# Kernel optimization log

Hardware: AMD Instinct MI355X
Metric: run time of the kernel (lower is better)

Reference implementation:

```python
import jax, jax.numpy as jnp
import numpy as np

STRIDES = (4, 8, 16, 32, 64)
SIZES = (32.0, 64.0, 128.0, 256.0, 512.0)
RATIOS = (0.5, 1.0, 2.0)
IM_H, IM_W = 1024, 1024
PRE_NMS = 1000
POST_NMS = 1000
IOU_THRESH = 0.7
MIN_SIZE = 0.0
SCALE_CLAMP = float(np.log(1000.0 / 16.0))  # detectron2 delta clamp


def _anchors(stride, size, H, W):
    # detectron2-style: area-preserving anchors centered on stride grid
    r = jnp.asarray(RATIOS, jnp.float32)
    w = jnp.sqrt(size * size / r)
    h = w * r
    base = jnp.stack([-w / 2, -h / 2, w / 2, h / 2], axis=1)  # [A,4]
    sx = jnp.arange(W, dtype=jnp.float32) * stride
    sy = jnp.arange(H, dtype=jnp.float32) * stride
    yy, xx = jnp.meshgrid(sy, sx, indexing='ij')
    shifts = jnp.stack([xx, yy, xx, yy], axis=-1).reshape(-1, 1, 4)  # [H*W,1,4]
    return (shifts + base[None]).reshape(-1, 4)  # [H*W*A, 4]


def _conv(x, w, b, pad):
    y = jax.lax.conv_general_dilated(
        x, w, (1, 1), [(pad, pad), (pad, pad)],
        dimension_numbers=('NCHW', 'OIHW', 'NCHW'))
    return y + b[None, :, None, None]


def _decode_clip(deltas, anchors):
    # deltas [N,M,4], anchors [1,M,4] -> clipped xyxy boxes [N,M,4]
    wa = anchors[..., 2] - anchors[..., 0]
    ha = anchors[..., 3] - anchors[..., 1]
    cxa = anchors[..., 0] + 0.5 * wa
    cya = anchors[..., 1] + 0.5 * ha
    dx, dy = deltas[..., 0], deltas[..., 1]
    dw = jnp.minimum(deltas[..., 2], SCALE_CLAMP)
    dh = jnp.minimum(deltas[..., 3], SCALE_CLAMP)
    cx = dx * wa + cxa
    cy = dy * ha + cya
    w = jnp.exp(dw) * wa
    h = jnp.exp(dh) * ha
    x1 = jnp.clip(cx - 0.5 * w, 0.0, float(IM_W))
    y1 = jnp.clip(cy - 0.5 * h, 0.0, float(IM_H))
    x2 = jnp.clip(cx + 0.5 * w, 0.0, float(IM_W))
    y2 = jnp.clip(cy + 0.5 * h, 0.0, float(IM_H))
    return jnp.stack([x1, y1, x2, y2], axis=-1)


def _iou_matrix(boxes):
    x1, y1, x2, y2 = boxes[:, 0], boxes[:, 1], boxes[:, 2], boxes[:, 3]
    area = (x2 - x1) * (y2 - y1)
    ix1 = jnp.maximum(x1[:, None], x1[None, :])
    iy1 = jnp.maximum(y1[:, None], y1[None, :])
    ix2 = jnp.minimum(x2[:, None], x2[None, :])
    iy2 = jnp.minimum(y2[:, None], y2[None, :])
    inter = jnp.clip(ix2 - ix1, 0.0) * jnp.clip(iy2 - iy1, 0.0)
    return inter / jnp.maximum(area[:, None] + area[None, :] - inter, 1e-6)


def _nms_keep(boxes):
    # boxes [M,4] already sorted by descending score; greedy NMS keep mask
    M = boxes.shape[0]
    valid = ((boxes[:, 2] - boxes[:, 0]) >= MIN_SIZE) & \
            ((boxes[:, 3] - boxes[:, 1]) >= MIN_SIZE)
    iou = _iou_matrix(boxes)
    idx = jnp.arange(M)

    def body(i, keep):
        sup = keep[i] & (iou[i] > IOU_THRESH) & (idx > i)
        return keep & ~sup

    return jax.lax.fori_loop(0, M, body, valid)


def _nms_single(boxes, scores):
    # boxes [PRE_NMS,4] score-sorted desc -> [POST_NMS,4], zero-padded
    del scores  # already sorted by score
    keep = _nms_keep(jax.lax.stop_gradient(boxes))
    order = jnp.argsort(~keep, stable=True)  # kept boxes first, score order preserved
    kept = keep[order][:POST_NMS]
    out = boxes[order[:POST_NMS]] * kept[:, None].astype(boxes.dtype)
    return out


def _rpn_forward(feats, conv_w, conv_b, obj_w, obj_b, delta_w, delta_b):
    N = feats[0].shape[0]
    A = len(RATIOS)
    boxes_all, scores_all = [], []
    for lvl, x in enumerate(feats):
        H, W = x.shape[2], x.shape[3]
        t = jax.nn.relu(_conv(x, conv_w, conv_b, 1))            # [N,256,H,W]
        logit = jax.nn.sigmoid(_conv(t, obj_w, obj_b, 0))       # [N,A,H,W]
        reg = _conv(t, delta_w, delta_b, 0)                     # [N,4A,H,W]
        scores = logit.transpose(0, 2, 3, 1).reshape(N, -1)     # [N,H*W*A]
        deltas = reg.reshape(N, A, 4, H, W).transpose(0, 3, 4, 1, 2).reshape(N, -1, 4)
        anchors = _anchors(STRIDES[lvl], SIZES[lvl], H, W)      # [H*W*A,4]
        rois = _decode_clip(deltas, anchors[None])              # [N,H*W*A,4]
        k = min(PRE_NMS, scores.shape[1])
        top_s, top_i = jax.lax.top_k(scores, k)
        boxes_all.append(jnp.take_along_axis(rois, top_i[..., None], axis=1))
        scores_all.append(top_s)
    boxes = jnp.concatenate(boxes_all, axis=1)   # [N,T,4]
    scores = jnp.concatenate(scores_all, axis=1)  # [N,T]
    top_s, top_i = jax.lax.top_k(scores, PRE_NMS)
    top_b = jnp.take_along_axis(boxes, top_i[..., None], axis=1)  # [N,PRE_NMS,4]
    dets = jax.vmap(_nms_single)(top_b, top_s)   # [N,POST_NMS,4]
    batch_inds = jnp.zeros((N, POST_NMS, 1), dets.dtype)
    ret = jnp.concatenate([batch_inds, dets], axis=2).reshape(-1, 5)
    return ret, dets.reshape(-1, 4)


def setup_inputs() -> dict:
    key = jax.random.key(0)
    ks = jax.random.split(key, 11)
    C = 256
    shapes = [(2, C, 256, 256), (2, C, 128, 128), (2, C, 64, 64),
              (2, C, 32, 32), (2, C, 16, 16)]
    inp = {}
    for i, (name, s) in enumerate(zip(['p2', 'p3', 'p4', 'p5', 'p6'], shapes)):
        inp[name] = jax.random.normal(ks[i], s, jnp.float32)
    inp['conv_w'] = jax.random.normal(ks[5], (C, C, 3, 3), jnp.float32) * 0.02
    inp['conv_b'] = jnp.zeros((C,), jnp.float32)
    inp['obj_w'] = jax.random.normal(ks[6], (3, C, 1, 1), jnp.float32) * 0.05
    inp['obj_b'] = jnp.zeros((3,), jnp.float32)
    inp['delta_w'] = jax.random.normal(ks[7], (12, C, 1, 1), jnp.float32) * 0.05
    inp['delta_b'] = jnp.zeros((12,), jnp.float32)
    return inp


def reference(p2, p3, p4, p5, p6, conv_w, conv_b, obj_w, obj_b, delta_w, delta_b):
    return _rpn_forward((p2, p3, p4, p5, p6), conv_w, conv_b,
                        obj_w, obj_b, delta_w, delta_b)
```

## Files before the change

kernel.cpp:

```cpp
#include <hip/hip_runtime.h>
#include <stdint.h>

typedef unsigned long long u64;
typedef unsigned int u32;
typedef _Float16 f16;
typedef _Float16 f16x8 __attribute__((ext_vector_type(8)));
typedef float f32x4 __attribute__((ext_vector_type(4)));
typedef u32 u32x4 __attribute__((ext_vector_type(4)));

#define NA 261888
#define CAP 4096
#define SCALE_CLAMP 4.135166556742356f
#define NBLK_IMG 684

#define WT_OFF   0
#define BOX_OFF  2359296
#define SB_OFF   10739712
#define HIST_OFF 12834816
#define FINE_OFF 12867584
#define META_OFF 13359104
#define CAND_OFF 13359168
#define TOP_OFF  13424704
#define MASK_OFF 13456704
#define NH_OFF   13712704
#define WS_NEED  192494912ull

#define E_WH   0
#define E_HB   3840
#define E_PART 3872
#define BUFB   26112

#define AS1C(p) ((const __attribute__((address_space(1))) void*)(p))
#define AS3(p)  ((__attribute__((address_space(3))) void*)(p))

__global__ void k_wprep(const float* __restrict__ w, f16* __restrict__ wHL) {
    int i = blockIdx.x * 256 + threadIdx.x;
    if (i >= 589824) return;
    int co = i / 2304, rem = i % 2304;
    int ci = rem / 9, kyx = rem % 9;
    float v = w[i];
    f16 h = (f16)v;
    f16 lo = (f16)(v - (float)h);
    u32 idx = (u32)((kyx * 32 + (ci >> 3)) * 256 + co) * 8 + (ci & 7);
    wHL[idx] = h;
    wHL[589824 + idx] = lo;
}

__global__ __launch_bounds__(256) void k_nhwc(
    const float* __restrict__ p2, const float* __restrict__ p3,
    const float* __restrict__ p4, const float* __restrict__ p5,
    const float* __restrict__ p6, unsigned char* __restrict__ nh)
{
    int t = blockIdx.x * 256 + threadIdx.x;
    if (t >= 1396736) return;
    int n = t / 698368;
    int r = t % 698368;
    int lvl, c, pxy, HW, cumpx;
    const float* in;
    if (r < 524288)      { lvl = 0; HW = 65536; cumpx = 0;     c = r >> 16; pxy = r & 65535; in = p2; }
    else if (r < 655360) { lvl = 1; HW = 16384; cumpx = 65536; r -= 524288; c = r >> 14; pxy = r & 16383; in = p3; }
    else if (r < 688128) { lvl = 2; HW = 4096;  cumpx = 81920; r -= 655360; c = r >> 12; pxy = r & 4095;  in = p4; }
    else if (r < 696320) { lvl = 3; HW = 1024;  cumpx = 86016; r -= 688128; c = r >> 10; pxy = r & 1023;  in = p5; }
    else                 { lvl = 4; HW = 256;   cumpx = 87040; r -= 696320; c = r >> 8;  pxy = r & 255;   in = p6; }
    (void)lvl;
    const float* gp = in + ((size_t)n * 256 + (size_t)c * 32) * HW + pxy;
    u32 hi[16], lo[16];
#pragma unroll
    for (int k = 0; k < 16; ++k) {
        float v0 = gp[(size_t)(2 * k) * HW];
        float v1 = gp[(size_t)(2 * k + 1) * HW];
        f16 h0 = (f16)v0, h1 = (f16)v1;
        f16 e0 = (f16)(v0 - (float)h0), e1 = (f16)(v1 - (float)h1);
        hi[k] = ((u32)__builtin_bit_cast(unsigned short, h1) << 16) |
                 (u32)__builtin_bit_cast(unsigned short, h0);
        lo[k] = ((u32)__builtin_bit_cast(unsigned short, e1) << 16) |
                 (u32)__builtin_bit_cast(unsigned short, e0);
    }
    unsigned char* dst = nh + ((size_t)n * 87296 + (size_t)cumpx) * 1024
                            + ((size_t)c * HW + (size_t)pxy) * 128;
    u32x4* d4 = (u32x4*)dst;
#pragma unroll
    for (int i = 0; i < 4; ++i)
        d4[i] = (u32x4){hi[4 * i], hi[4 * i + 1], hi[4 * i + 2], hi[4 * i + 3]};
#pragma unroll
    for (int i = 0; i < 4; ++i)
        d4[4 + i] = (u32x4){lo[4 * i], lo[4 * i + 1], lo[4 * i + 2], lo[4 * i + 3]};
}

__global__ __launch_bounds__(256, 2) void k_conv_nh(
    const unsigned char* __restrict__ nh, const f16* __restrict__ wHL,
    const float* __restrict__ cb, const float* __restrict__ ow,
    const float* __restrict__ ob, const float* __restrict__ dw_,
    const float* __restrict__ db_, u32* __restrict__ scoreb,
    float* __restrict__ boxes)
{
    __shared__ __align__(16) float smf[13056];
    char* smemc = (char*)smf;

    int tid = threadIdx.x;
    int bid = blockIdx.x;
    int ebid = (bid & 7) * 171 + (bid >> 3);
    int n = ebid / NBLK_IMG;
    int tb = ebid % NBLK_IMG;
    int lvl, t0, cumpx;
    if      (tb < 512) { lvl = 0; t0 = tb;       cumpx = 0;     }
    else if (tb < 640) { lvl = 1; t0 = tb - 512; cumpx = 65536; }
    else if (tb < 672) { lvl = 2; t0 = tb - 640; cumpx = 81920; }
    else if (tb < 680) { lvl = 3; t0 = tb - 672; cumpx = 86016; }
    else               { lvl = 4; t0 = tb - 680; cumpx = 87040; }
    int H = 256 >> lvl, W = H;
    int HW = H * W;
    int xtiles = (W >= 32) ? (W >> 5) : 1;
    int xt = t0 % xtiles, yt = t0 / xtiles;
    int tx0 = xt * 32, ty0 = yt * 4;
    const unsigned char* nhb = nh + ((size_t)n * 87296 + (size_t)cumpx) * 1024;

    int l = tid & 63;
    int wid = tid >> 6;
    int wm = wid >> 1, wn = wid & 1;
    int lr = l & 15;
    int lg = l >> 4;

    int srco[7];
#pragma unroll
    for (int w = 0; w < 7; ++w) {
        int flat = w * 256 + tid;
        int px = flat >> 3, seg = flat & 7;
        int dy = px / 34, dx = px % 34;
        int y = ty0 + dy - 1, x = tx0 + dx - 1;
        bool part = flat < 1632;
        bool inb = part && y >= 0 && y < H && x >= 0 && x < W;
        srco[w] = inb ? ((y * W + x) * 128 + ((seg * 16) ^ ((px & 7) << 4))) : -1;
    }

#pragma unroll
    for (int w = 0; w < 7; ++w) {
        int flat = w * 256 + tid;
        if (flat < 1632 && srco[w] < 0) {
            *(u32x4*)(smemc + flat * 16) = (u32x4){0u, 0u, 0u, 0u};
            *(u32x4*)(smemc + BUFB + flat * 16) = (u32x4){0u, 0u, 0u, 0u};
        }
    }

    f32x4 acc[4][8];
#pragma unroll
    for (int mi = 0; mi < 4; ++mi)
#pragma unroll
        for (int nf = 0; nf < 8; ++nf) acc[mi][nf] = (f32x4){0.f, 0.f, 0.f, 0.f};

    const f16* wHp = wHL;
    const f16* wLp = wHL + 589824;

#pragma unroll
    for (int w = 0; w < 7; ++w)
        if (srco[w] >= 0)
            __builtin_amdgcn_global_load_lds(AS1C(nhb + srco[w]),
                AS3(smemc + (w * 256 + (tid & ~63)) * 16), 16, 0, 0);
    __syncthreads();

    for (int chunk = 0; chunk < 8; ++chunk) {
        if (chunk < 7) {
            const unsigned char* cb2 = nhb + (size_t)(chunk + 1) * HW * 128;
            int nb = ((chunk + 1) & 1) * BUFB;
#pragma unroll
            for (int w = 0; w < 7; ++w)
                if (srco[w] >= 0)
                    __builtin_amdgcn_global_load_lds(AS1C(cb2 + srco[w]),
                        AS3(smemc + nb + (w * 256 + (tid & ~63)) * 16), 16, 0, 0);
        }
        int cb_ = (chunk & 1) * BUFB;

        for (int kyx = 0; kyx < 9; ++kyx) {
            int ky = kyx / 3, kx = kyx % 3;
            f16x8 aH[4], aL[4];
#pragma unroll
            for (int mi = 0; mi < 4; ++mi) {
                int q = (2 * wm + (mi >> 1) + ky) * 34 + (mi & 1) * 16 + kx + lr;
                int sw = (q & 7) << 4;
                int rb = cb_ + q * 128;
                aH[mi] = *(const f16x8*)(smemc + rb + ((lg * 16) ^ sw));
                aL[mi] = *(const f16x8*)(smemc + rb + ((64 + lg * 16) ^ sw));
            }
            u32 kbase = (u32)(kyx * 32 + chunk * 4 + lg) * 256;
#pragma unroll
            for (int h = 0; h < 2; ++h) {
                f16x8 bH[4], bL[4];
#pragma unroll
                for (int j = 0; j < 4; ++j) {
                    int nf = h * 4 + j;
                    u32 ei = (kbase + (u32)(wn * 128 + nf * 16 + lr)) * 8;
                    bH[j] = *(const f16x8*)(wHp + ei);
                    bL[j] = *(const f16x8*)(wLp + ei);
                }
#pragma unroll
                for (int j = 0; j < 4; ++j) {
#pragma unroll
                    for (int mi = 0; mi < 4; ++mi) {
                        f32x4 c = acc[mi][h * 4 + j];
                        c = __builtin_amdgcn_mfma_f32_16x16x32_f16(aH[mi], bH[j], c, 0, 0, 0);
                        c = __builtin_amdgcn_mfma_f32_16x16x32_f16(aH[mi], bL[j], c, 0, 0, 0);
                        c = __builtin_amdgcn_mfma_f32_16x16x32_f16(aL[mi], bH[j], c, 0, 0, 0);
                        acc[mi][h * 4 + j] = c;
                    }
                }
            }
        }
        __syncthreads();
    }

    for (int j = tid; j < 3840; j += 256) {
        int o = j >> 8, co = j & 255;
        smf[E_WH + j] = (o < 3) ? ow[o * 256 + co] : dw_[(o - 3) * 256 + co];
    }
    if (tid < 15) smf[E_HB + tid] = (tid < 3) ? ob[tid] : db_[tid - 3];
    for (int j = tid; j < 1920; j += 256) smf[E_PART + j] = 0.f;

    float cbv[8];
#pragma unroll
    for (int nf = 0; nf < 8; ++nf) cbv[nf] = cb[wn * 128 + nf * 16 + lr];
    __syncthreads();

#pragma unroll
    for (int mi = 0; mi < 4; ++mi)
#pragma unroll
        for (int nf = 0; nf < 8; ++nf)
#pragma unroll
            for (int e = 0; e < 4; ++e)
                acc[mi][nf][e] = fmaxf(acc[mi][nf][e] + cbv[nf], 0.f);

    for (int o = 0; o < 15; ++o) {
        float wv[8];
#pragma unroll
        for (int nf = 0; nf < 8; ++nf) wv[nf] = smf[E_WH + o * 256 + wn * 128 + nf * 16 + lr];
#pragma unroll
        for (int mi = 0; mi < 4; ++mi) {
#pragma unroll
            for (int e = 0; e < 4; ++e) {
                float s = 0.f;
#pragma unroll
                for (int nf = 0; nf < 8; ++nf) s = fmaf(wv[nf], acc[mi][nf][e], s);
                s += __shfl_xor(s, 1);
                s += __shfl_xor(s, 2);
// ... 15 lines not shown
            int aOff = (lvl == 0) ? 0 : (lvl == 1) ? 196608 : (lvl == 2) ? 245760 : (lvl == 3) ? 258048 : 261120;
            float size = (float)(32 << lvl);
            float stride = (float)(4 << lvl);
            float cxa = gx * stride, cya = gy * stride;
#pragma unroll
            for (int a = 0; a < 3; ++a) {
                float lgt = smf[E_PART + (wm * 15 + a) * 64 + px] + smf[E_HB + a];
                float dxv = smf[E_PART + (wm * 15 + 3 + a * 4 + 0) * 64 + px] + smf[E_HB + 3 + a * 4 + 0];
                float dyv = smf[E_PART + (wm * 15 + 3 + a * 4 + 1) * 64 + px] + smf[E_HB + 3 + a * 4 + 1];
                float dwv = smf[E_PART + (wm * 15 + 3 + a * 4 + 2) * 64 + px] + smf[E_HB + 3 + a * 4 + 2];
                float dhv = smf[E_PART + (wm * 15 + 3 + a * 4 + 3) * 64 + px] + smf[E_HB + 3 + a * 4 + 3];
                float r = (a == 0) ? 0.5f : (a == 1) ? 1.0f : 2.0f;
                float wa = sqrtf(size * size / r);
                float ha = wa * r;
                dwv = fminf(dwv, SCALE_CLAMP);
                dhv = fminf(dhv, SCALE_CLAMP);
                float cx = dxv * wa + cxa, cy = dyv * ha + cya;
                float w_ = expf(dwv) * wa, h_ = expf(dhv) * ha;
                float x1 = fminf(fmaxf(cx - 0.5f * w_, 0.f), 1024.f);
                float y1 = fminf(fmaxf(cy - 0.5f * h_, 0.f), 1024.f);
                float x2 = fminf(fmaxf(cx + 0.5f * w_, 0.f), 1024.f);
                float y2 = fminf(fmaxf(cy + 0.5f * h_, 0.f), 1024.f);
                double sc = 1.0 / (1.0 + exp(-(double)lgt));
                u32 bits = __float_as_uint((float)sc);
                int gi = aOff + (gy * W + gx) * 3 + a;
                scoreb[(size_t)n * NA + gi] = bits;
                float* bp = boxes + ((size_t)n * NA + gi) * 4;
                bp[0] = x1; bp[1] = y1; bp[2] = x2; bp[3] = y2;
            }
        }
    }
}

__global__ __launch_bounds__(256, 2) void k_conv_legacy(
    const float* __restrict__ p2, const float* __restrict__ p3,
    const float* __restrict__ p4, const float* __restrict__ p5,
    const float* __restrict__ p6, const f16* __restrict__ wHL,
    const float* __restrict__ cb, const float* __restrict__ ow,
    const float* __restrict__ ob, const float* __restrict__ dw_,
    const float* __restrict__ db_, u32* __restrict__ scoreb,
    float* __restrict__ boxes)
{
    __shared__ __align__(16) float smf[6528];
    char* smemc = (char*)smf;

    int tid = threadIdx.x;
    int bid = blockIdx.x;
    int n = bid / NBLK_IMG;
    int tb = bid % NBLK_IMG;
    int lvl, t0;
    if      (tb < 512) { lvl = 0; t0 = tb;       }
    else if (tb < 640) { lvl = 1; t0 = tb - 512; }
    else if (tb < 672) { lvl = 2; t0 = tb - 640; }
    else if (tb < 680) { lvl = 3; t0 = tb - 672; }
    else               { lvl = 4; t0 = tb - 680; }
    int H = 256 >> lvl, W = H;
    int HW = H * W;
    int xtiles = (W >= 32) ? (W >> 5) : 1;
    int xt = t0 % xtiles, yt = t0 / xtiles;
    int tx0 = xt * 32, ty0 = yt * 4;
    const float* in = (lvl == 0) ? p2 : (lvl == 1) ? p3 : (lvl == 2) ? p4 : (lvl == 3) ? p5 : p6;
    in += (size_t)n * 256 * HW;

    int l = tid & 63;
    int wid = tid >> 6;
    int wm = wid >> 1, wn = wid & 1;
    int lr = l & 15;
    int lg = l >> 4;

    int off[13];
#pragma unroll
    for (int w = 0; w < 13; ++w) {
        int idx = w * 256 + tid;
        int ci2 = idx / 204, p = idx % 204;
        int dy = p / 34, dx = p % 34;
        int y = ty0 + dy - 1, x = tx0 + dx - 1;
        bool inb = (idx < 3264) && y >= 0 && y < H && x >= 0 && x < W;
        off[w] = inb ? (ci2 * 2 * HW + y * W + x) : -1;
    }

    float rv0[13], rv1[13];
#pragma unroll
    for (int w = 0; w < 13; ++w) {
        rv0[w] = 0.f; rv1[w] = 0.f;
        if (off[w] >= 0) { const float* gp = in + off[w]; rv0[w] = gp[0]; rv1[w] = gp[HW]; }
    }

    f32x4 acc[4][8];
#pragma unroll
    for (int mi = 0; mi < 4; ++mi)
#pragma unroll
        for (int nf = 0; nf < 8; ++nf) acc[mi][nf] = (f32x4){0.f, 0.f, 0.f, 0.f};

    const f16* wHp = wHL;
    const f16* wLp = wHL + 589824;

    for (int chunk = 0; chunk < 8; ++chunk) {
        __syncthreads();
#pragma unroll
        for (int w = 0; w < 13; ++w) {
            int idx = w * 256 + tid;
            if (idx < 3264) {
                int ci2 = idx / 204, p = idx % 204;
                f16 h0 = (f16)rv0[w], h1 = (f16)rv1[w];
                f16 e0 = (f16)(rv0[w] - (float)h0), e1 = (f16)(rv1[w] - (float)h1);
                u32 hp = ((u32)__builtin_bit_cast(unsigned short, h1) << 16) |
                          (u32)__builtin_bit_cast(unsigned short, h0);
                u32 lp = ((u32)__builtin_bit_cast(unsigned short, e1) << 16) |
                          (u32)__builtin_bit_cast(unsigned short, e0);
                int sw = (p & 7) << 4;
                int rb = p * 128;
                *(u32*)(smemc + rb + ((ci2 * 4) ^ sw)) = hp;
                *(u32*)(smemc + rb + ((64 + ci2 * 4) ^ sw)) = lp;
            }
        }
        if (chunk < 7) {
            const float* cbase = in + (size_t)(chunk + 1) * 32 * HW;
#pragma unroll
            for (int w = 0; w < 13; ++w) {
                rv0[w] = 0.f; rv1[w] = 0.f;
                if (off[w] >= 0) { const float* gp = cbase + off[w]; rv0[w] = gp[0]; rv1[w] = gp[HW]; }
            }
        }
        __syncthreads();

        for (int kyx = 0; kyx < 9; ++kyx) {
            int ky = kyx / 3, kx = kyx % 3;
            f16x8 aH[4], aL[4];
#pragma unroll
            for (int mi = 0; mi < 4; ++mi) {
                int q = (2 * wm + (mi >> 1) + ky) * 34 + (mi & 1) * 16 + kx + lr;
                int sw = (q & 7) << 4;
                int rb = q * 128;
                aH[mi] = *(const f16x8*)(smemc + rb + ((lg * 16) ^ sw));
                aL[mi] = *(const f16x8*)(smemc + rb + ((64 + lg * 16) ^ sw));
            }
            u32 kbase = (u32)(kyx * 32 + chunk * 4 + lg) * 256;
#pragma unroll
            for (int h = 0; h < 2; ++h) {
                f16x8 bH[4], bL[4];
#pragma unroll
                for (int j = 0; j < 4; ++j) {
                    int nf = h * 4 + j;
                    u32 ei = (kbase + (u32)(wn * 128 + nf * 16 + lr)) * 8;
                    bH[j] = *(const f16x8*)(wHp + ei);
                    bL[j] = *(const f16x8*)(wLp + ei);
                }
#pragma unroll
                for (int j = 0; j < 4; ++j) {
#pragma unroll
                    for (int mi = 0; mi < 4; ++mi) {
                        f32x4 c = acc[mi][h * 4 + j];
                        c = __builtin_amdgcn_mfma_f32_16x16x32_f16(aH[mi], bH[j], c, 0, 0, 0);
                        c = __builtin_amdgcn_mfma_f32_16x16x32_f16(aH[mi], bL[j], c, 0, 0, 0);
                        c = __builtin_amdgcn_mfma_f32_16x16x32_f16(aL[mi], bH[j], c, 0, 0, 0);
                        acc[mi][h * 4 + j] = c;
                    }
                }
            }
        }
    }

    __syncthreads();
    for (int j = tid; j < 3840; j += 256) {
        int o = j >> 8, co = j & 255;
        smf[E_WH + j] = (o < 3) ? ow[o * 256 + co] : dw_[(o - 3) * 256 + co];
    }
    if (tid < 15) smf[E_HB + tid] = (tid < 3) ? ob[tid] : db_[tid - 3];
    for (int j = tid; j < 1920; j += 256) smf[E_PART + j] = 0.f;

    float cbv[8];
#pragma unroll
    for (int nf = 0; nf < 8; ++nf) cbv[nf] = cb[wn * 128 + nf * 16 + lr];
    __syncthreads();

#pragma unroll
    for (int mi = 0; mi < 4; ++mi)
#pragma unroll
        for (int nf = 0; nf < 8; ++nf)
#pragma unroll
            for (int e = 0; e < 4; ++e)
                acc[mi][nf][e] = fmaxf(acc[mi][nf][e] + cbv[nf], 0.f);

    for (int o = 0; o < 15; ++o) {
        float wv[8];
#pragma unroll
        for (int nf = 0; nf < 8; ++nf) wv[nf] = smf[E_WH + o * 256 + wn * 128 + nf * 16 + lr];
#pragma unroll
        for (int mi = 0; mi < 4; ++mi) {
#pragma unroll
            for (int e = 0; e < 4; ++e) {
                float s = 0.f;
#pragma unroll
                for (int nf = 0; nf < 8; ++nf) s = fmaf(wv[nf], acc[mi][nf][e], s);
                s += __shfl_xor(s, 1);
                s += __shfl_xor(s, 2);
                s += __shfl_xor(s, 4);
                s += __shfl_xor(s, 8);
                if (lr == 0)
                    atomicAdd(&smf[E_PART + (wm * 15 + o) * 64 + mi * 16 + lg * 4 + e], s);
            }
        }
    }
    __syncthreads();

    if ((l & 63) < 32) {
        int px = wn * 32 + (l & 31);
        int yy = 2 * wm + (px >> 5);
        int gx = tx0 + (px & 31);
        int gy = ty0 + yy;
        if (gx < W) {
            int aOff = (lvl == 0) ? 0 : (lvl == 1) ? 196608 : (lvl == 2) ? 245760 : (lvl == 3) ? 258048 : 261120;
            float size = (float)(32 << lvl);
            float stride = (float)(4 << lvl);
            float cxa = gx * stride, cya = gy * stride;
#pragma unroll
            for (int a = 0; a < 3; ++a) {
                float lgt = smf[E_PART + (wm * 15 + a) * 64 + px] + smf[E_HB + a];
                float dxv = smf[E_PART + (wm * 15 + 3 + a * 4 + 0) * 64 + px] + smf[E_HB + 3 + a * 4 + 0];
                float dyv = smf[E_PART + (wm * 15 + 3 + a * 4 + 1) * 64 + px] + smf[E_HB + 3 + a * 4 + 1];
                float dwv = smf[E_PART + (wm * 15 + 3 + a * 4 + 2) * 64 + px] + smf[E_HB + 3 + a * 4 + 2];
                float dhv = smf[E_PART + (wm * 15 + 3 + a * 4 + 3) * 64 + px] + smf[E_HB + 3 + a * 4 + 3];
                float r = (a == 0) ? 0.5f : (a == 1) ? 1.0f : 2.0f;
                float wa = sqrtf(size * size / r);
                float ha = wa * r;
                dwv = fminf(dwv, SCALE_CLAMP);
                dhv = fminf(dhv, SCALE_CLAMP);
                float cx = dxv * wa + cxa, cy = dyv * ha + cya;
                float w_ = expf(dwv) * wa, h_ = expf(dhv) * ha;
                float x1 = fminf(fmaxf(cx - 0.5f * w_, 0.f), 1024.f);
                float y1 = fminf(fmaxf(cy - 0.5f * h_, 0.f), 1024.f);
                float x2 = fminf(fmaxf(cx + 0.5f * w_, 0.f), 1024.f);
                float y2 = fminf(fmaxf(cy + 0.5f * h_, 0.f), 1024.f);
                double sc = 1.0 / (1.0 + exp(-(double)lgt));
                u32 bits = __float_as_uint((float)sc);
                int gi = aOff + (gy * W + gx) * 3 + a;
                scoreb[(size_t)n * NA + gi] = bits;
                float* bp = boxes + ((size_t)n * NA + gi) * 4;
                bp[0] = x1; bp[1] = y1; bp[2] = x2; bp[3] = y2;
            }
        }
    }
}

__global__ __launch_bounds__(256) void k_histc(const u32* __restrict__ scoreb,
                                               u32* __restrict__ histc) {
    __shared__ u32 lh[4096];
    for (int j = threadIdx.x; j < 4096; j += 256) lh[j] = 0;
    __syncthreads();
    int n = blockIdx.x >> 6;
    int blk = blockIdx.x & 63;
    const u32* sb = scoreb + (size_t)n * NA;
    for (int i = blk * 256 + threadIdx.x; i < NA; i += 64 * 256)
        atomicAdd(&lh[sb[i] >> 20], 1u);
    __syncthreads();
    for (int j = threadIdx.x; j < 4096; j += 256) {
        u32 v = lh[j];
        if (v) atomicAdd(&histc[n * 4096 + j], v);
    }
}

__global__ void k_scanc(const u32* __restrict__ histc, u32* __restrict__ meta) {
    int n = blockIdx.x, tid = threadIdx.x;
    __shared__ u32 cs[256];
    u32 s = 0;
    for (int j = 0; j < 16; ++j) s += histc[n * 4096 + (4095 - (tid * 16 + j))];
    cs[tid] = s;
    __syncthreads();
    if (tid == 0) {
        u32 cum = 0;
        for (int t = 0; t < 256; ++t) {
            if (cum + cs[t] >= 1000u) {
                u32 c2 = cum;
                for (int d = t * 16;; ++d) {
                    int bin = 4095 - d;
                    u32 h = histc[n * 4096 + bin];
                    if (c2 + h >= 1000u) { meta[n * 4 + 1] = (u32)bin; meta[n * 4 + 2] = c2; break; }
                    c2 += h;
                }
                break;
            }
            cum += cs[t];
        }
    }
}

__global__ void k_fine(const u32* __restrict__ scoreb, const u32* __restrict__ meta,
                       u32* __restrict__ fineh) {
    __shared__ u32 lf[32];
    if (threadIdx.x < 32) lf[threadIdx.x] = 0;
    __syncthreads();
    u32 C0 = meta[1], C1 = meta[5];
    int stridex = gridDim.x * blockDim.x;
    for (int i = blockIdx.x * blockDim.x + threadIdx.x; i < 2 * NA; i += stridex) {
        u32 b = scoreb[i];
        int n = (i >= NA);
        if ((b >> 20) == (n ? C1 : C0)) atomicAdd(&lf[n * 16 + ((b >> 16) & 15)], 1u);
    }
    __syncthreads();
    if (threadIdx.x < 32) {
        u32 v = lf[threadIdx.x];
        if (v) atomicAdd(&fineh[threadIdx.x], v);
    }
}

__global__ void k_scanf(const u32* __restrict__ fineh, u32* __restrict__ meta) {
    int n = threadIdx.x;
    if (n < 2) {
        u32 cum = meta[n * 4 + 2];
        u32 C = meta[n * 4 + 1];
        u32 T = C << 4;
        for (int f = 15; f >= 0; --f) {
            cum += fineh[n * 16 + f];
            if (cum >= 1000u) { T = (C << 4) | (u32)f; break; }
        }
        meta[n * 4] = T;
    }
}

__global__ void k_compact(const u32* __restrict__ scoreb, const u32* __restrict__ meta,
                          u32* __restrict__ cnt, u64* __restrict__ cand) {
    int stridex = gridDim.x * blockDim.x;
    for (int i = blockIdx.x * blockDim.x + threadIdx.x; i < 2 * NA; i += stridex) {
        u32 b = scoreb[i];
        int n = (i >= NA);
        u32 T = meta[n * 4];
        if ((b >> 16) >= T) {
            u32 p = atomicAdd(&cnt[n], 1u);
            if (p < CAP)
                cand[n * CAP + p] = ((u64)(~b) << 32) | (u32)(i - n * NA);
        }
    }
}

__global__ __launch_bounds__(1024) void k_sort(const u64* __restrict__ cand,
                                               const u32* __restrict__ cnt,
                                               const float* __restrict__ boxes,
                                               float* __restrict__ topbox) {
    __shared__ u64 a[CAP];
    int n = blockIdx.x, tid = threadIdx.x;
    u32 C = cnt[n]; if (C > CAP) C = CAP;
    for (int i = tid; i < CAP; i += 1024)
        a[i] = (i < (int)C) ? cand[n * CAP + i] : ~0ULL;
    __syncthreads();
    for (int k = 2; k <= CAP; k <<= 1) {
        for (int j = k >> 1; j > 0; j >>= 1) {
            for (int i = tid; i < CAP; i += 1024) {
                int l = i ^ j;
                if (l > i) {
// ... 86 lines not shown
        const float* bp = topbox + (n * 1000 + i) * 4;
        float x1 = kept ? bp[0] : 0.f;
        float y1 = kept ? bp[1] : 0.f;
        float x2 = kept ? bp[2] : 0.f;
        float y2 = kept ? bp[3] : 0.f;
        size_t rrow = (size_t)n * 1000 + pos;
        out[rrow * 5 + 0] = 0.f;
        out[rrow * 5 + 1] = x1; out[rrow * 5 + 2] = y1;
        out[rrow * 5 + 3] = x2; out[rrow * 5 + 4] = y2;
        float* dp = out + 10000 + rrow * 4;
        dp[0] = x1; dp[1] = y1; dp[2] = x2; dp[3] = y2;
    }
}

extern "C" void kernel_launch(void* const* d_in, const int* in_sizes, int n_in,
                              void* d_out, int out_size, void* d_ws, size_t ws_size,
                              hipStream_t stream) {
    const float* p2 = (const float*)d_in[0];
    const float* p3 = (const float*)d_in[1];
    const float* p4 = (const float*)d_in[2];
    const float* p5 = (const float*)d_in[3];
    const float* p6 = (const float*)d_in[4];
    const float* conv_w = (const float*)d_in[5];
    const float* conv_b = (const float*)d_in[6];
    const float* obj_w = (const float*)d_in[7];
    const float* obj_b = (const float*)d_in[8];
    const float* delta_w = (const float*)d_in[9];
    const float* delta_b = (const float*)d_in[10];
    char* ws = (char*)d_ws;

    f16*   wHL    = (f16*)  (ws + WT_OFF);
    float* boxes  = (float*)(ws + BOX_OFF);
    u32*   scoreb = (u32*)  (ws + SB_OFF);
    u32*   histc  = (u32*)  (ws + HIST_OFF);
    u32*   fineh  = (u32*)  (ws + FINE_OFF);
    u32*   meta   = (u32*)  (ws + META_OFF);
    u32*   cnt    = meta + 8;
    u64*   cand   = (u64*)  (ws + CAND_OFF);
    float* topbox = (float*)(ws + TOP_OFF);
    u64*   mask   = (u64*)  (ws + MASK_OFF);

    hipMemsetAsync(ws + HIST_OFF, 0, 32768 + 128, stream);
    hipMemsetAsync(ws + META_OFF, 0, 64, stream);

    k_wprep<<<2304, 256, 0, stream>>>(conv_w, wHL);

    if (ws_size >= WS_NEED) {
        unsigned char* nh = (unsigned char*)(ws + NH_OFF);
        k_nhwc<<<5456, 256, 0, stream>>>(p2, p3, p4, p5, p6, nh);
        k_conv_nh<<<2 * NBLK_IMG, 256, 0, stream>>>(nh, wHL, conv_b,
                                                    obj_w, obj_b, delta_w, delta_b,
                                                    scoreb, boxes);
    } else {
        k_conv_legacy<<<2 * NBLK_IMG, 256, 0, stream>>>(p2, p3, p4, p5, p6, wHL, conv_b,
                                                        obj_w, obj_b, delta_w, delta_b,
                                                        scoreb, boxes);
    }
    k_histc<<<128, 256, 0, stream>>>(scoreb, histc);
    k_scanc<<<2, 256, 0, stream>>>(histc, meta);
    k_fine<<<512, 256, 0, stream>>>(scoreb, meta, fineh);
    k_scanf<<<1, 64, 0, stream>>>(fineh, meta);
    k_compact<<<1024, 256, 0, stream>>>(scoreb, meta, cnt, cand);
    k_sort<<<2, 1024, 0, stream>>>(cand, cnt, boxes, topbox);
    k_mask<<<8, 256, 0, stream>>>(topbox, mask);
    k_final<<<2, 256, 0, stream>>>(topbox, mask, (float*)d_out);
    (void)in_sizes; (void)n_in; (void)out_size; (void)ws_size;
}
```

Measured before the change: 1.056 ms.

## Fuse score histogram into conv epilogue and single-buffer NHWC LDS tile

The conv kernel now atomically adds each score's top 16 bits into a global 65536-bin histogram. That removes the separate coarse histogram, fine histogram and two scan kernels, which are replaced by one 16-bit-radix scan. The NHWC conv path also drops LDS double buffering, halving shared memory to allow higher occupancy, but it now waits on each chunk load behind syncs. MFMA sections gain s_setprio raises. The risks are global atomic contention on histogram bins, the loss of load/compute overlap, and a larger histogram memset.

```diff
diff --git a/kernel.cpp b/kernel.cpp
--- a/kernel.cpp
+++ b/kernel.cpp
@@ -17,7 +17,6 @@
 #define BOX_OFF  2359296
 #define SB_OFF   10739712
 #define HIST_OFF 12834816
-#define FINE_OFF 12867584
 #define META_OFF 13359104
 #define CAND_OFF 13359168
 #define TOP_OFF  13424704
@@ -28,7 +27,6 @@
 #define E_WH   0
 #define E_HB   3840
 #define E_PART 3872
-#define BUFB   26112
 
 #define AS1C(p) ((const __attribute__((address_space(1))) void*)(p))
 #define AS3(p)  ((__attribute__((address_space(3))) void*)(p))
@@ -92,9 +90,9 @@
     const float* __restrict__ cb, const float* __restrict__ ow,
     const float* __restrict__ ob, const float* __restrict__ dw_,
     const float* __restrict__ db_, u32* __restrict__ scoreb,
-    float* __restrict__ boxes)
+    float* __restrict__ boxes, u32* __restrict__ hist)
 {
-    __shared__ __align__(16) float smf[13056];
+    __shared__ __align__(16) float smf[6528];
     char* smemc = (char*)smf;
 
     int tid = threadIdx.x;
@@ -136,10 +134,8 @@
 #pragma unroll
     for (int w = 0; w < 7; ++w) {
         int flat = w * 256 + tid;
-        if (flat < 1632 && srco[w] < 0) {
+        if (flat < 1632 && srco[w] < 0)
             *(u32x4*)(smemc + flat * 16) = (u32x4){0u, 0u, 0u, 0u};
-            *(u32x4*)(smemc + BUFB + flat * 16) = (u32x4){0u, 0u, 0u, 0u};
-        }
     }
 
     f32x4 acc[4][8];
@@ -151,24 +147,15 @@
     const f16* wHp = wHL;
     const f16* wLp = wHL + 589824;
 
-#pragma unroll
-    for (int w = 0; w < 7; ++w)
-        if (srco[w] >= 0)
-            __builtin_amdgcn_global_load_lds(AS1C(nhb + srco[w]),
-                AS3(smemc + (w * 256 + (tid & ~63)) * 16), 16, 0, 0);
-    __syncthreads();
-
     for (int chunk = 0; chunk < 8; ++chunk) {
-        if (chunk < 7) {
-            const unsigned char* cb2 = nhb + (size_t)(chunk + 1) * HW * 128;
-            int nb = ((chunk + 1) & 1) * BUFB;
-#pragma unroll
-            for (int w = 0; w < 7; ++w)
-                if (srco[w] >= 0)
-                    __builtin_amdgcn_global_load_lds(AS1C(cb2 + srco[w]),
-                        AS3(smemc + nb + (w * 256 + (tid & ~63)) * 16), 16, 0, 0);
-        }
-        int cb_ = (chunk & 1) * BUFB;
+        __syncthreads();
+        const unsigned char* cb2 = nhb + (size_t)chunk * HW * 128;
+#pragma unroll
+        for (int w = 0; w < 7; ++w)
+            if (srco[w] >= 0)
+                __builtin_amdgcn_global_load_lds(AS1C(cb2 + srco[w]),
+                    AS3(smemc + (w * 256 + (tid & ~63)) * 16), 16, 0, 0);
+        __syncthreads();
 
         for (int kyx = 0; kyx < 9; ++kyx) {
             int ky = kyx / 3, kx = kyx % 3;
@@ -177,7 +164,7 @@
             for (int mi = 0; mi < 4; ++mi) {
                 int q = (2 * wm + (mi >> 1) + ky) * 34 + (mi & 1) * 16 + kx + lr;
                 int sw = (q & 7) << 4;
-                int rb = cb_ + q * 128;
+                int rb = q * 128;
                 aH[mi] = *(const f16x8*)(smemc + rb + ((lg * 16) ^ sw));
                 aL[mi] = *(const f16x8*)(smemc + rb + ((64 + lg * 16) ^ sw));
             }
@@ -192,6 +179,7 @@
                     bH[j] = *(const f16x8*)(wHp + ei);
                     bL[j] = *(const f16x8*)(wLp + ei);
                 }
+                __builtin_amdgcn_s_setprio(1);
 #pragma unroll
                 for (int j = 0; j < 4; ++j) {
 #pragma unroll
@@ -203,11 +191,224 @@
                         acc[mi][h * 4 + j] = c;
                     }
                 }
-            }
-        }
+                __builtin_amdgcn_s_setprio(0);
+            }
+        }
+    }
+
+    __syncthreads();
+    for (int j = tid; j < 3840; j += 256) {
+        int o = j >> 8, co = j & 255;
+        smf[E_WH + j] = (o < 3) ? ow[o * 256 + co] : dw_[(o - 3) * 256 + co];
+    }
+    if (tid < 15) smf[E_HB + tid] = (tid < 3) ? ob[tid] : db_[tid - 3];
+    for (int j = tid; j < 1920; j += 256) smf[E_PART + j] = 0.f;
+
+    float cbv[8];
+#pragma unroll
+    for (int nf = 0; nf < 8; ++nf) cbv[nf] = cb[wn * 128 + nf * 16 + lr];
+    __syncthreads();
+
+#pragma unroll
+    for (int mi = 0; mi < 4; ++mi)
+#pragma unroll
+        for (int nf = 0; nf < 8; ++nf)
+#pragma unroll
+            for (int e = 0; e < 4; ++e)
+                acc[mi][nf][e] = fmaxf(acc[mi][nf][e] + cbv[nf], 0.f);
+
+    for (int o = 0; o < 15; ++o) {
+        float wv[8];
+#pragma unroll
+        for (int nf = 0; nf < 8; ++nf) wv[nf] = smf[E_WH + o * 256 + wn * 128 + nf * 16 + lr];
+#pragma unroll
+        for (int mi = 0; mi < 4; ++mi) {
+#pragma unroll
+            for (int e = 0; e < 4; ++e) {
+                float s = 0.f;
+#pragma unroll
+                for (int nf = 0; nf < 8; ++nf) s = fmaf(wv[nf], acc[mi][nf][e], s);
+                s += __shfl_xor(s, 1);
+                s += __shfl_xor(s, 2);
+                s += __shfl_xor(s, 4);
+                s += __shfl_xor(s, 8);
+                if (lr == 0)
+                    atomicAdd(&smf[E_PART + (wm * 15 + o) * 64 + mi * 16 + lg * 4 + e], s);
+            }
+        }
+    }
+    __syncthreads();
+
+    if ((l & 63) < 32) {
+        int px = wn * 32 + (l & 31);
+        int yy = 2 * wm + (px >> 5);
+        int gx = tx0 + (px & 31);
+        int gy = ty0 + yy;
+        if (gx < W) {
+            int aOff = (lvl == 0) ? 0 : (lvl == 1) ? 196608 : (lvl == 2) ? 245760 : (lvl == 3) ? 258048 : 261120;
+            float size = (float)(32 << lvl);
+            float stride = (float)(4 << lvl);
+            float cxa = gx * stride, cya = gy * stride;
+#pragma unroll
+            for (int a = 0; a < 3; ++a) {
+                float lgt = smf[E_PART + (wm * 15 + a) * 64 + px] + smf[E_HB + a];
+                float dxv = smf[E_PART + (wm * 15 + 3 + a * 4 + 0) * 64 + px] + smf[E_HB + 3 + a * 4 + 0];
+                float dyv = smf[E_PART + (wm * 15 + 3 + a * 4 + 1) * 64 + px] + smf[E_HB + 3 + a * 4 + 1];
+                float dwv = smf[E_PART + (wm * 15 + 3 + a * 4 + 2) * 64 + px] + smf[E_HB + 3 + a * 4 + 2];
+                float dhv = smf[E_PART + (wm * 15 + 3 + a * 4 + 3) * 64 + px] + smf[E_HB + 3 + a * 4 + 3];
+                float r = (a == 0) ? 0.5f : (a == 1) ? 1.0f : 2.0f;
+                float wa = sqrtf(size * size / r);
+                float ha = wa * r;
+                dwv = fminf(dwv, SCALE_CLAMP);
+                dhv = fminf(dhv, SCALE_CLAMP);
+                float cx = dxv * wa + cxa, cy = dyv * ha + cya;
+                float w_ = expf(dwv) * wa, h_ = expf(dhv) * ha;
+                float x1 = fminf(fmaxf(cx - 0.5f * w_, 0.f), 1024.f);
+                float y1 = fminf(fmaxf(cy - 0.5f * h_, 0.f), 1024.f);
+                float x2 = fminf(fmaxf(cx + 0.5f * w_, 0.f), 1024.f);
+                float y2 = fminf(fmaxf(cy + 0.5f * h_, 0.f), 1024.f);
+                double sc = 1.0 / (1.0 + exp(-(double)lgt));
+                u32 bits = __float_as_uint((float)sc);
+                int gi = aOff + (gy * W + gx) * 3 + a;
+                scoreb[(size_t)n * NA + gi] = bits;
+                atomicAdd(&hist[n * 65536 + (bits >> 16)], 1u);
+                float* bp = boxes + ((size_t)n * NA + gi) * 4;
+                bp[0] = x1; bp[1] = y1; bp[2] = x2; bp[3] = y2;
+            }
+        }
+    }
+}
+
+__global__ __launch_bounds__(256, 2) void k_conv_legacy(
+    const float* __restrict__ p2, const float* __restrict__ p3,
+    const float* __restrict__ p4, const float* __restrict__ p5,
+    const float* __restrict__ p6, const f16* __restrict__ wHL,
+    const float* __restrict__ cb, const float* __restrict__ ow,
+    const float* __restrict__ ob, const float* __restrict__ dw_,
+    const float* __restrict__ db_, u32* __restrict__ scoreb,
+    float* __restrict__ boxes)
+{
+    __shared__ __align__(16) float smf[6528];
+    char* smemc = (char*)smf;
+
+    int tid = threadIdx.x;
+    int bid = blockIdx.x;
+    int n = bid / NBLK_IMG;
+    int tb = bid % NBLK_IMG;
+    int lvl, t0;
+    if      (tb < 512) { lvl = 0; t0 = tb;       }
+    else if (tb < 640) { lvl = 1; t0 = tb - 512; }
+    else if (tb < 672) { lvl = 2; t0 = tb - 640; }
+    else if (tb < 680) { lvl = 3; t0 = tb - 672; }
+    else               { lvl = 4; t0 = tb - 680; }
+    int H = 256 >> lvl, W = H;
+    int HW = H * W;
+    int xtiles = (W >= 32) ? (W >> 5) : 1;
+    int xt = t0 % xtiles, yt = t0 / xtiles;
+    int tx0 = xt * 32, ty0 = yt * 4;
+    const float* in = (lvl == 0) ? p2 : (lvl == 1) ? p3 : (lvl == 2) ? p4 : (lvl == 3) ? p5 : p6;
+    in += (size_t)n * 256 * HW;
+
+    int l = tid & 63;
+    int wid = tid >> 6;
+    int wm = wid >> 1, wn = wid & 1;
+    int lr = l & 15;
+    int lg = l >> 4;
+
+    int off[13];
+#pragma unroll
+    for (int w = 0; w < 13; ++w) {
+        int idx = w * 256 + tid;
+        int ci2 = idx / 204, p = idx % 204;
+        int dy = p / 34, dx = p % 34;
+        int y = ty0 + dy - 1, x = tx0 + dx - 1;
+        bool inb = (idx < 3264) && y >= 0 && y < H && x >= 0 && x < W;
+        off[w] = inb ? (ci2 * 2 * HW + y * W + x) : -1;
+    }
+
+    float rv0[13], rv1[13];
+#pragma unroll
+    for (int w = 0; w < 13; ++w) {
+        rv0[w] = 0.f; rv1[w] = 0.f;
+        if (off[w] >= 0) { const float* gp = in + off[w]; rv0[w] = gp[0]; rv1[w] = gp[HW]; }
+    }
+
+    f32x4 acc[4][8];
+#pragma unroll
+    for (int mi = 0; mi < 4; ++mi)
+#pragma unroll
+        for (int nf = 0; nf < 8; ++nf) acc[mi][nf] = (f32x4){0.f, 0.f, 0.f, 0.f};
+
+    const f16* wHp = wHL;
+    const f16* wLp = wHL + 589824;
+
+    for (int chunk = 0; chunk < 8; ++chunk) {
         __syncthreads();
-    }
-
+#pragma unroll
+        for (int w = 0; w < 13; ++w) {
+            int idx = w * 256 + tid;
+            if (idx < 3264) {
+                int ci2 = idx / 204, p = idx % 204;
+                f16 h0 = (f16)rv0[w], h1 = (f16)rv1[w];
+                f16 e0 = (f16)(rv0[w] - (float)h0), e1 = (f16)(rv1[w] - (float)h1);
+                u32 hp = ((u32)__builtin_bit_cast(unsigned short, h1) << 16) |
+                          (u32)__builtin_bit_cast(unsigned short, h0);
+                u32 lp = ((u32)__builtin_bit_cast(unsigned short, e1) << 16) |
+                          (u32)__builtin_bit_cast(unsigned short, e0);
+                int sw = (p & 7) << 4;
+                int rb = p * 128;
+                *(u32*)(smemc + rb + ((ci2 * 4) ^ sw)) = hp;
+                *(u32*)(smemc + rb + ((64 + ci2 * 4) ^ sw)) = lp;
+            }
+        }
+        if (chunk < 7) {
+            const float* cbase = in + (size_t)(chunk + 1) * 32 * HW;
+#pragma unroll
+            for (int w = 0; w < 13; ++w) {
+                rv0[w] = 0.f; rv1[w] = 0.f;
+                if (off[w] >= 0) { const float* gp = cbase + off[w]; rv0[w] = gp[0]; rv1[w] = gp[HW]; }
+            }
+        }
+        __syncthreads();
+
+        for (int kyx = 0; kyx < 9; ++kyx) {
+            int ky = kyx / 3, kx = kyx % 3;
+            f16x8 aH[4], aL[4];
+#pragma unroll
+            for (int mi = 0; mi < 4; ++mi) {
+                int q = (2 * wm + (mi >> 1) + ky) * 34 + (mi & 1) * 16 + kx + lr;
+                int sw = (q & 7) << 4;
+                int rb = q * 128;
+                aH[mi] = *(const f16x8*)(smemc + rb + ((lg * 16) ^ sw));
+                aL[mi] = *(const f16x8*)(smemc + rb + ((64 + lg * 16) ^ sw));
+            }
+            u32 kbase = (u32)(kyx * 32 + chunk * 4 + lg) * 256;
+#pragma unroll
+            for (int h = 0; h < 2; ++h) {
+                f16x8 bH[4], bL[4];
+#pragma unroll
+                for (int j = 0; j < 4; ++j) {
+                    int nf = h * 4 + j;
+                    u32 ei = (kbase + (u32)(wn * 128 + nf * 16 + lr)) * 8;
+                    bH[j] = *(const f16x8*)(wHp + ei);
+                    bL[j] = *(const f16x8*)(wLp + ei);
+                }
+#pragma unroll
+                for (int j = 0; j < 4; ++j) {
+#pragma unroll
+                    for (int mi = 0; mi < 4; ++mi) {
+                        f32x4 c = acc[mi][h * 4 + j];
+                        c = __builtin_amdgcn_mfma_f32_16x16x32_f16(aH[mi], bH[j], c, 0, 0, 0);
+                        c = __builtin_amdgcn_mfma_f32_16x16x32_f16(aH[mi], bL[j], c, 0, 0, 0);
+                        c = __builtin_amdgcn_mfma_f32_16x16x32_f16(aL[mi], bH[j], c, 0, 0, 0);
+                        acc[mi][h * 4 + j] = c;
+                    }
+                }
+            }
+        }
+    }
+
+    __syncthreads();
     for (int j = tid; j < 3840; j += 256) {
         int o = j >> 8, co = j & 255;
         smf[E_WH + j] = (o < 3) ? ow[o * 256 + co] : dw_[(o - 3) * 256 + co];
@@ -289,289 +490,38 @@
     }
 }
 
-__global__ __launch_bounds__(256, 2) void k_conv_legacy(
-    const float* __restrict__ p2, const float* __restrict__ p3,
-    const float* __restrict__ p4, const float* __restrict__ p5,
-    const float* __restrict__ p6, const f16* __restrict__ wHL,
-    const float* __restrict__ cb, const float* __restrict__ ow,
-    const float* __restrict__ ob, const float* __restrict__ dw_,
-    const float* __restrict__ db_, u32* __restrict__ scoreb,
-    float* __restrict__ boxes)
-{
-    __shared__ __align__(16) float smf[6528];
-    char* smemc = (char*)smf;
-
-    int tid = threadIdx.x;
-    int bid = blockIdx.x;
-    int n = bid / NBLK_IMG;
-    int tb = bid % NBLK_IMG;
-    int lvl, t0;
-    if      (tb < 512) { lvl = 0; t0 = tb;       }
-    else if (tb < 640) { lvl = 1; t0 = tb - 512; }
-    else if (tb < 672) { lvl = 2; t0 = tb - 640; }
-    else if (tb < 680) { lvl = 3; t0 = tb - 672; }
-    else               { lvl = 4; t0 = tb - 680; }
-    int H = 256 >> lvl, W = H;
-    int HW = H * W;
-    int xtiles = (W >= 32) ? (W >> 5) : 1;
-    int xt = t0 % xtiles, yt = t0 / xtiles;
-    int tx0 = xt * 32, ty0 = yt * 4;
-    const float* in = (lvl == 0) ? p2 : (lvl == 1) ? p3 : (lvl == 2) ? p4 : (lvl == 3) ? p5 : p6;
-    in += (size_t)n * 256 * HW;
-
-    int l = tid & 63;
-    int wid = tid >> 6;
-    int wm = wid >> 1, wn = wid & 1;
-    int lr = l & 15;
-    int lg = l >> 4;
-
-    int off[13];
-#pragma unroll
-    for (int w = 0; w < 13; ++w) {
-        int idx = w * 256 + tid;
-        int ci2 = idx / 204, p = idx % 204;
-        int dy = p / 34, dx = p % 34;
-        int y = ty0 + dy - 1, x = tx0 + dx - 1;
-        bool inb = (idx < 3264) && y >= 0 && y < H && x >= 0 && x < W;
-        off[w] = inb ? (ci2 * 2 * HW + y * W + x) : -1;
-    }
-
-    float rv0[13], rv1[13];
-#pragma unroll
-    for (int w = 0; w < 13; ++w) {
-        rv0[w] = 0.f; rv1[w] = 0.f;
-        if (off[w] >= 0) { const float* gp = in + off[w]; rv0[w] = gp[0]; rv1[w] = gp[HW]; }
-    }
-
-    f32x4 acc[4][8];
-#pragma unroll
-    for (int mi = 0; mi < 4; ++mi)
-#pragma unroll
-        for (int nf = 0; nf < 8; ++nf) acc[mi][nf] = (f32x4){0.f, 0.f, 0.f, 0.f};
-
-    const f16* wHp = wHL;
-    const f16* wLp = wHL + 589824;
-
-    for (int chunk = 0; chunk < 8; ++chunk) {
-        __syncthreads();
-#pragma unroll
-        for (int w = 0; w < 13; ++w) {
-            int idx = w * 256 + tid;
-            if (idx < 3264) {
-                int ci2 = idx / 204, p = idx % 204;
-                f16 h0 = (f16)rv0[w], h1 = (f16)rv1[w];
-                f16 e0 = (f16)(rv0[w] - (float)h0), e1 = (f16)(rv1[w] - (float)h1);
-                u32 hp = ((u32)__builtin_bit_cast(unsigned short, h1) << 16) |
-                          (u32)__builtin_bit_cast(unsigned short, h0);
-                u32 lp = ((u32)__builtin_bit_cast(unsigned short, e1) << 16) |
-                          (u32)__builtin_bit_cast(unsigned short, e0);
-                int sw = (p & 7) << 4;
-                int rb = p * 128;
-                *(u32*)(smemc + rb + ((ci2 * 4) ^ sw)) = hp;
-                *(u32*)(smemc + rb + ((64 + ci2 * 4) ^ sw)) = lp;
-            }
-        }
-        if (chunk < 7) {
-            const float* cbase = in + (size_t)(chunk + 1) * 32 * HW;
-#pragma unroll
-            for (int w = 0; w < 13; ++w) {
-                rv0[w] = 0.f; rv1[w] = 0.f;
-                if (off[w] >= 0) { const float* gp = cbase + off[w]; rv0[w] = gp[0]; rv1[w] = gp[HW]; }
-            }
-        }
-        __syncthreads();
-
-        for (int kyx = 0; kyx < 9; ++kyx) {
-            int ky = kyx / 3, kx = kyx % 3;
-            f16x8 aH[4], aL[4];
-#pragma unroll
-            for (int mi = 0; mi < 4; ++mi) {
-                int q = (2 * wm + (mi >> 1) + ky) * 34 + (mi & 1) * 16 + kx + lr;
-                int sw = (q & 7) << 4;
-                int rb = q * 128;
-                aH[mi] = *(const f16x8*)(smemc + rb + ((lg * 16) ^ sw));
-                aL[mi] = *(const f16x8*)(smemc + rb + ((64 + lg * 16) ^ sw));
-            }
-            u32 kbase = (u32)(kyx * 32 + chunk * 4 + lg) * 256;
-#pragma unroll
-            for (int h = 0; h < 2; ++h) {
-                f16x8 bH[4], bL[4];
-#pragma unroll
-                for (int j = 0; j < 4; ++j) {
-                    int nf = h * 4 + j;
-                    u32 ei = (kbase + (u32)(wn * 128 + nf * 16 + lr)) * 8;
-                    bH[j] = *(const f16x8*)(wHp + ei);
-                    bL[j] = *(const f16x8*)(wLp + ei);
-                }
-#pragma unroll
-                for (int j = 0; j < 4; ++j) {
-#pragma unroll
-                    for (int mi = 0; mi < 4; ++mi) {
-                        f32x4 c = acc[mi][h * 4 + j];
-                        c = __builtin_amdgcn_mfma_f32_16x16x32_f16(aH[mi], bH[j], c, 0, 0, 0);
-                        c = __builtin_amdgcn_mfma_f32_16x16x32_f16(aH[mi], bL[j], c, 0, 0, 0);
-                        c = __builtin_amdgcn_mfma_f32_16x16x32_f16(aL[mi], bH[j], c, 0, 0, 0);
-                        acc[mi][h * 4 + j] = c;
-                    }
-                }
-            }
-        }
-    }
-
-    __syncthreads();
-    for (int j = tid; j < 3840; j += 256) {
-        int o = j >> 8, co = j & 255;
-        smf[E_WH + j] = (o < 3) ? ow[o * 256 + co] : dw_[(o - 3) * 256 + co];
-    }
-    if (tid < 15) smf[E_HB + tid] = (tid < 3) ? ob[tid] : db_[tid - 3];
-    for (int j = tid; j < 1920; j += 256) smf[E_PART + j] = 0.f;
-
-    float cbv[8];
-#pragma unroll
-    for (int nf = 0; nf < 8; ++nf) cbv[nf] = cb[wn * 128 + nf * 16 + lr];
-    __syncthreads();
-
-#pragma unroll
-    for (int mi = 0; mi < 4; ++mi)
-#pragma unroll
-        for (int nf = 0; nf < 8; ++nf)
-#pragma unroll
-            for (int e = 0; e < 4; ++e)
-                acc[mi][nf][e] = fmaxf(acc[mi][nf][e] + cbv[nf], 0.f);
-
-    for (int o = 0; o < 15; ++o) {
-        float wv[8];
-#pragma unroll
-        for (int nf = 0; nf < 8; ++nf) wv[nf] = smf[E_WH + o * 256 + wn * 128 + nf * 16 + lr];
-#pragma unroll
-        for (int mi = 0; mi < 4; ++mi) {
-#pragma unroll
-            for (int e = 0; e < 4; ++e) {
-                float s = 0.f;
-#pragma unroll
-                for (int nf = 0; nf < 8; ++nf) s = fmaf(wv[nf], acc[mi][nf][e], s);
-                s += __shfl_xor(s, 1);
-                s += __shfl_xor(s, 2);
-                s += __shfl_xor(s, 4);
-                s += __shfl_xor(s, 8);
-                if (lr == 0)
-                    atomicAdd(&smf[E_PART + (wm * 15 + o) * 64 + mi * 16 + lg * 4 + e], s);
-            }
-        }
-    }
-    __syncthreads();
-
-    if ((l & 63) < 32) {
-        int px = wn * 32 + (l & 31);
-        int yy = 2 * wm + (px >> 5);
-        int gx = tx0 + (px & 31);
-        int gy = ty0 + yy;
-        if (gx < W) {
-            int aOff = (lvl == 0) ? 0 : (lvl == 1) ? 196608 : (lvl == 2) ? 245760 : (lvl == 3) ? 258048 : 261120;
-            float size = (float)(32 << lvl);
-            float stride = (float)(4 << lvl);
-            float cxa = gx * stride, cya = gy * stride;
-#pragma unroll
-            for (int a = 0; a < 3; ++a) {
-                float lgt = smf[E_PART + (wm * 15 + a) * 64 + px] + smf[E_HB + a];
-                float dxv = smf[E_PART + (wm * 15 + 3 + a * 4 + 0) * 64 + px] + smf[E_HB + 3 + a * 4 + 0];
-                float dyv = smf[E_PART + (wm * 15 + 3 + a * 4 + 1) * 64 + px] + smf[E_HB + 3 + a * 4 + 1];
-                float dwv = smf[E_PART + (wm * 15 + 3 + a * 4 + 2) * 64 + px] + smf[E_HB + 3 + a * 4 + 2];
-                float dhv = smf[E_PART + (wm * 15 + 3 + a * 4 + 3) * 64 + px] + smf[E_HB + 3 + a * 4 + 3];
-                float r = (a == 0) ? 0.5f : (a == 1) ? 1.0f : 2.0f;
-                float wa = sqrtf(size * size / r);
-                float ha = wa * r;
-                dwv = fminf(dwv, SCALE_CLAMP);
-                dhv = fminf(dhv, SCALE_CLAMP);
-                float cx = dxv * wa + cxa, cy = dyv * ha + cya;
-                float w_ = expf(dwv) * wa, h_ = expf(dhv) * ha;
-                float x1 = fminf(fmaxf(cx - 0.5f * w_, 0.f), 1024.f);
-                float y1 = fminf(fmaxf(cy - 0.5f * h_, 0.f), 1024.f);
-                float x2 = fminf(fmaxf(cx + 0.5f * w_, 0.f), 1024.f);
-                float y2 = fminf(fmaxf(cy + 0.5f * h_, 0.f), 1024.f);
-                double sc = 1.0 / (1.0 + exp(-(double)lgt));
-                u32 bits = __float_as_uint((float)sc);
-                int gi = aOff + (gy * W + gx) * 3 + a;
-                scoreb[(size_t)n * NA + gi] = bits;
-                float* bp = boxes + ((size_t)n * NA + gi) * 4;
-                bp[0] = x1; bp[1] = y1; bp[2] = x2; bp[3] = y2;
-            }
-        }
-    }
-}
-
-__global__ __launch_bounds__(256) void k_histc(const u32* __restrict__ scoreb,
-                                               u32* __restrict__ histc) {
-    __shared__ u32 lh[4096];
-    for (int j = threadIdx.x; j < 4096; j += 256) lh[j] = 0;
-    __syncthreads();
-    int n = blockIdx.x >> 6;
-    int blk = blockIdx.x & 63;
-    const u32* sb = scoreb + (size_t)n * NA;
-    for (int i = blk * 256 + threadIdx.x; i < NA; i += 64 * 256)
-        atomicAdd(&lh[sb[i] >> 20], 1u);
-    __syncthreads();
-    for (int j = threadIdx.x; j < 4096; j += 256) {
-        u32 v = lh[j];
-        if (v) atomicAdd(&histc[n * 4096 + j], v);
-    }
-}
-
-__global__ void k_scanc(const u32* __restrict__ histc, u32* __restrict__ meta) {
-    int n = blockIdx.x, tid = threadIdx.x;
-    __shared__ u32 cs[256];
-    u32 s = 0;
-    for (int j = 0; j < 16; ++j) s += histc[n * 4096 + (4095 - (tid * 16 + j))];
-    cs[tid] = s;
-    __syncthreads();
-    if (tid == 0) {
-        u32 cum = 0;
-        for (int t = 0; t < 256; ++t) {
-            if (cum + cs[t] >= 1000u) {
-                u32 c2 = cum;
-                for (int d = t * 16;; ++d) {
-                    int bin = 4095 - d;
-                    u32 h = histc[n * 4096 + bin];
-                    if (c2 + h >= 1000u) { meta[n * 4 + 1] = (u32)bin; meta[n * 4 + 2] = c2; break; }
-                    c2 += h;
-                }
-                break;
-            }
-            cum += cs[t];
-        }
-    }
-}
-
-__global__ void k_fine(const u32* __restrict__ scoreb, const u32* __restrict__ meta,
-                       u32* __restrict__ fineh) {
-    __shared__ u32 lf[32];
-    if (threadIdx.x < 32) lf[threadIdx.x] = 0;
-    __syncthreads();
-    u32 C0 = meta[1], C1 = meta[5];
+__global__ void k_hist(const u32* __restrict__ scoreb, u32* __restrict__ hist) {
     int stridex = gridDim.x * blockDim.x;
     for (int i = blockIdx.x * blockDim.x + threadIdx.x; i < 2 * NA; i += stridex) {
         u32 b = scoreb[i];
         int n = (i >= NA);
-        if ((b >> 20) == (n ? C1 : C0)) atomicAdd(&lf[n * 16 + ((b >> 16) & 15)], 1u);
-    }
-    __syncthreads();
-    if (threadIdx.x < 32) {
-        u32 v = lf[threadIdx.x];
-        if (v) atomicAdd(&fineh[threadIdx.x], v);
-    }
-}
-
-__global__ void k_scanf(const u32* __restrict__ fineh, u32* __restrict__ meta) {
-    int n = threadIdx.x;
-    if (n < 2) {
-        u32 cum = meta[n * 4 + 2];
-        u32 C = meta[n * 4 + 1];
-        u32 T = C << 4;
-        for (int f = 15; f >= 0; --f) {
-            cum += fineh[n * 16 + f];
-            if (cum >= 1000u) { T = (C << 4) | (u32)f; break; }
-        }
-        meta[n * 4] = T;
+        atomicAdd(&hist[n * 65536 + (b >> 16)], 1u);
+    }
+}
+
+__global__ void k_scan(const u32* __restrict__ hist, u32* __restrict__ meta) {
+    int n = blockIdx.x, tid = threadIdx.x;
+    __shared__ u32 cs[256];
+    u32 s = 0;
+    for (int d = tid * 256; d < tid * 256 + 256; ++d)
+        s += hist[n * 65536 + (65535 - d)];
+    cs[tid] = s;
+    __syncthreads();
+    if (tid == 0) {
+        u32 cum = 0; int T = 0;
+        for (int t = 0; t < 256; ++t) {
+            if (cum + cs[t] >= 1000u) {
+                u32 c2 = cum;
+                for (int d = t * 256;; ++d) {
+                    int bin = 65535 - d;
+                    c2 += hist[n * 65536 + bin];
+                    if (c2 >= 1000u) { T = bin; break; }
+                }
+                break;
+            }
+            cum += cs[t];
+        }
+        meta[n * 4] = (u32)T;
     }
 }
 
@@ -724,16 +674,14 @@
     f16*   wHL    = (f16*)  (ws + WT_OFF);
     float* boxes  = (float*)(ws + BOX_OFF);
     u32*   scoreb = (u32*)  (ws + SB_OFF);
-    u32*   histc  = (u32*)  (ws + HIST_OFF);
-    u32*   fineh  = (u32*)  (ws + FINE_OFF);
+    u32*   hist   = (u32*)  (ws + HIST_OFF);
     u32*   meta   = (u32*)  (ws + META_OFF);
     u32*   cnt    = meta + 8;
     u64*   cand   = (u64*)  (ws + CAND_OFF);
     float* topbox = (float*)(ws + TOP_OFF);
     u64*   mask   = (u64*)  (ws + MASK_OFF);
 
-    hipMemsetAsync(ws + HIST_OFF, 0, 32768 + 128, stream);
-    hipMemsetAsync(ws + META_OFF, 0, 64, stream);
+    hipMemsetAsync(ws + HIST_OFF, 0, 524288 + 64, stream);
 
     k_wprep<<<2304, 256, 0, stream>>>(conv_w, wHL);
 
@@ -742,16 +690,14 @@
         k_nhwc<<<5456, 256, 0, stream>>>(p2, p3, p4, p5, p6, nh);
         k_conv_nh<<<2 * NBLK_IMG, 256, 0, stream>>>(nh, wHL, conv_b,
                                                     obj_w, obj_b, delta_w, delta_b,
-                                                    scoreb, boxes);
+                                                    scoreb, boxes, hist);
     } else {
         k_conv_legacy<<<2 * NBLK_IMG, 256, 0, stream>>>(p2, p3, p4, p5, p6, wHL, conv_b,
                                                         obj_w, obj_b, delta_w, delta_b,
                                                         scoreb, boxes);
-    }
-    k_histc<<<128, 256, 0, stream>>>(scoreb, histc);
-    k_scanc<<<2, 256, 0, stream>>>(histc, meta);
-    k_fine<<<512, 256, 0, stream>>>(scoreb, meta, fineh);
-    k_scanf<<<1, 64, 0, stream>>>(fineh, meta);
+        k_hist<<<1024, 256, 0, stream>>>(scoreb, hist);
+    }
+    k_scan<<<2, 256, 0, stream>>>(hist, meta);
     k_compact<<<1024, 256, 0, stream>>>(scoreb, meta, cnt, cand);
     k_sort<<<2, 1024, 0, stream>>>(cand, cnt, boxes, topbox);
     k_mask<<<8, 256, 0, stream>>>(topbox, mask);
```

Measured after the change: 1.142 ms. 8.2% more time.
